# Kernel optimization log

Hardware: AMD Instinct MI355X
Metric: run time of the kernel (lower is better)

## Reference

```python
import jax, jax.numpy as jnp
import numpy as np

B, S, H, DH = 4, 1024, 8, 64
D = H * DH
CLIP_K = 5
NUM_RPR = 2 * CLIP_K + 1  # 11


def setup_inputs() -> dict:
    key = jax.random.key(0)
    ks = jax.random.split(key, 12)
    w_scale = 0.01  # truncated_normal stddev approx
    inp = {
        'q': jax.random.normal(ks[0], (B, S, D), jnp.float32),
        'k': jax.random.normal(ks[1], (B, S, D), jnp.float32),
        'v': jax.random.normal(ks[2], (B, S, D), jnp.float32),
        'rpr_matrix': jax.random.randint(ks[3], (S, S), 0, NUM_RPR, jnp.int32),
        'wq_kernel': jax.random.normal(ks[4], (D, D), jnp.float32) * w_scale,
        'wq_bias': jnp.zeros((D,), jnp.float32),
        'wk_kernel': jax.random.normal(ks[5], (D, D), jnp.float32) * w_scale,
        'wk_bias': jnp.zeros((D,), jnp.float32),
        'wv_kernel': jax.random.normal(ks[6], (D, D), jnp.float32) * w_scale,
        'wv_bias': jnp.zeros((D,), jnp.float32),
        'krpr': jax.random.normal(ks[7], (NUM_RPR, DH), jnp.float32),
    }
    return inp


def reference(q, k, v, rpr_matrix, wq_kernel, wq_bias, wk_kernel, wk_bias,
              wv_kernel, wv_bias, krpr):
    b, s, d = q.shape
    dh = krpr.shape[-1]
    h = d // dh

    def proj(x, w, bias):
        # [B,S,D] -> [B,H,S,DH]
        y = x.reshape(-1, d) @ w + bias
        return y.reshape(b, s, h, dh).transpose(0, 2, 1, 3)

    qh = proj(q, wq_kernel, wq_bias)
    kh = proj(k, wk_kernel, wk_bias)
    vh = proj(v, wv_kernel, wv_bias)

    # standard QK^T scores
    scores = jnp.einsum('bhqd,bhkd->bhqk', qh, kh)
    # RPR key bias: gather per-relative-position key embeddings (note: original
    # code uses krpr for BOTH the key-side and value-side RPR; vrpr is unused)
    alpha = krpr[rpr_matrix]  # [Sq, Sk, DH]
    scores = scores + jnp.einsum('bhqd,qkd->bhqk', qh, alpha)
    scores = scores / jnp.sqrt(jnp.float32(dh))

    probs = jax.nn.softmax(scores, axis=-1)

    ctx = jnp.einsum('bhqk,bhkd->bhqd', probs, vh)
    ctx = ctx + jnp.einsum('bhqk,qkd->bhqd', probs, alpha)

    # [B,H,S,DH] -> [B,S,D]
    return ctx.transpose(0, 2, 1, 3).reshape(b, s, d)
```

## Files before the change

### kernel.cpp

```cpp
#include <hip/hip_runtime.h>

typedef unsigned short u16;
typedef unsigned int u32;
typedef __attribute__((ext_vector_type(8))) short short8;
typedef __attribute__((ext_vector_type(4))) float f32x4;

__device__ __forceinline__ float bf2f(u16 v) {
  return __uint_as_float(((unsigned)v) << 16);
}
__device__ __forceinline__ u16 f2bf(float f) {
  unsigned u = __float_as_uint(f);
  return (u16)((u + 0x7fffu + ((u >> 16) & 1u)) >> 16);
}
__device__ __forceinline__ u32 pk2(float lo, float hi) {
  return (u32)f2bf(lo) | ((u32)f2bf(hi) << 16);
}

__device__ __forceinline__ float ld1in(const void* p, size_t i, bool f32) {
  return f32 ? ((const float*)p)[i] : bf2f(((const u16*)p)[i]);
}
__device__ __forceinline__ float4 ld4in(const void* p, size_t i, bool f32) {
  if (f32) return *(const float4*)((const float*)p + i);
  ushort4 u = *(const ushort4*)((const u16*)p + i);
  return make_float4(bf2f(u.x), bf2f(u.y), bf2f(u.z), bf2f(u.w));
}
__device__ __forceinline__ void ld8in(const void* p, size_t i, bool f32, float* v) {
  if (f32) {
    float4 a = *(const float4*)((const float*)p + i);
    float4 b = *(const float4*)((const float*)p + i + 4);
    v[0] = a.x; v[1] = a.y; v[2] = a.z; v[3] = a.w;
    v[4] = b.x; v[5] = b.y; v[6] = b.z; v[7] = b.w;
  } else {
    ushort4 a = *(const ushort4*)((const u16*)p + i);
    ushort4 b = *(const ushort4*)((const u16*)p + i + 4);
    v[0] = bf2f(a.x); v[1] = bf2f(a.y); v[2] = bf2f(a.z); v[3] = bf2f(a.w);
    v[4] = bf2f(b.x); v[5] = bf2f(b.y); v[6] = bf2f(b.z); v[7] = bf2f(b.w);
  }
}

__device__ __forceinline__ void st1ws(float* p, size_t i, float v) { p[i] = v; }
__device__ __forceinline__ void st1ws(u16* p, size_t i, float v) { p[i] = f2bf(v); }
__device__ __forceinline__ float4 ld4ws(const float* p, size_t i) { return *(const float4*)(p + i); }
__device__ __forceinline__ float4 ld4ws(const u16* p, size_t i) {
  ushort4 u = *(const ushort4*)(p + i);
  return make_float4(bf2f(u.x), bf2f(u.y), bf2f(u.z), bf2f(u.w));
}
template <typename WT>
__device__ __forceinline__ uint4 ld8ws_pk(const WT* p, size_t i) {
  float4 a = ld4ws(p, i), b = ld4ws(p, i + 4);
  uint4 r;
  r.x = pk2(a.x, a.y); r.y = pk2(a.z, a.w);
  r.z = pk2(b.x, b.y); r.w = pk2(b.z, b.w);
  return r;
}
template <>
__device__ __forceinline__ uint4 ld8ws_pk<u16>(const u16* p, size_t i) {
  return *(const uint4*)(p + i);
}


__global__ void rpr_detect_kernel(const u16* __restrict__ q, int* __restrict__ flag) {
  __shared__ int cnt[256];
  int t = threadIdx.x, c = 0;
  for (int i = t; i < 8192; i += 256) {
    unsigned e = (q[i] >> 7) & 0xff;
    c += (e >= 0xC0) ? 1 : 0;
  }
  cnt[t] = c;
  __syncthreads();
  if (t == 0) {
    int s = 0;
    for (int i = 0; i < 256; ++i) s += cnt[i];
    *flag = (s > 128) ? 1 : 0;
  }
}

template <typename WT>
__global__ __launch_bounds__(256, 2) void rpr_proj_mfma(
    const void* __restrict__ xq, const void* __restrict__ xk, const void* __restrict__ xv,
    const void* __restrict__ wqp, const void* __restrict__ wkp, const void* __restrict__ wvp,
    const void* __restrict__ bqp, const void* __restrict__ bkp, const void* __restrict__ bvp,
    WT* __restrict__ ws, const int* __restrict__ flagp) {
  const bool f32 = (*flagp != 0);
  const int z = blockIdx.z;
  const void* __restrict__ X = (z == 0) ? xq : (z == 1) ? xk : xv;
  const void* __restrict__ W = (z == 0) ? wqp : (z == 1) ? wkp : wvp;
  const void* __restrict__ Bb = (z == 0) ? bqp : (z == 1) ? bkp : bvp;
  WT* __restrict__ O = ws + (size_t)z * (4096u * 512u);

  __shared__ u32 as32[64][20];
  __shared__ u32 bs32[64][20];

  const int t = threadIdx.x;
  const int wvi = t >> 6, lane = t & 63;
  const int quad = lane >> 4, col = lane & 15;
  const int m0 = blockIdx.y * 64, n0 = blockIdx.x * 64;

  f32x4 acc[4] = {{0.f, 0.f, 0.f, 0.f}, {0.f, 0.f, 0.f, 0.f},
                  {0.f, 0.f, 0.f, 0.f}, {0.f, 0.f, 0.f, 0.f}};

  for (int k0 = 0; k0 < 512; k0 += 32) {
    {
      int m = t >> 2, kc = (t & 3) * 8;
      float v[8];
      ld8in(X, (size_t)(m0 + m) * 512 + k0 + kc, f32, v);
      uint4 pk;
      pk.x = pk2(v[0], v[1]); pk.y = pk2(v[2], v[3]);
      pk.z = pk2(v[4], v[5]); pk.w = pk2(v[6], v[7]);
      *(uint4*)&as32[m][(t & 3) * 4] = pk;
    }
    {
      int kp = t & 15, nb = (t >> 4) * 4;
      float4 r0 = ld4in(W, (size_t)(k0 + 2 * kp) * 512 + n0 + nb, f32);
      float4 r1 = ld4in(W, (size_t)(k0 + 2 * kp + 1) * 512 + n0 + nb, f32);
      bs32[nb + 0][kp] = pk2(r0.x, r1.x);
      bs32[nb + 1][kp] = pk2(r0.y, r1.y);
      bs32[nb + 2][kp] = pk2(r0.z, r1.z);
      bs32[nb + 3][kp] = pk2(r0.w, r1.w);
    }
    __syncthreads();
    short8 aF = *(const short8*)((const u16*)&as32[wvi * 16 + col][0] + quad * 8);
#pragma unroll
    for (int c = 0; c < 4; ++c) {
      short8 bF = *(const short8*)((const u16*)&bs32[c * 16 + col][0] + quad * 8);
      acc[c] = __builtin_amdgcn_mfma_f32_16x16x32_bf16(aF, bF, acc[c], 0, 0, 0);
    }
    __syncthreads();
  }

  const int h = blockIdx.x;
#pragma unroll
  for (int c = 0; c < 4; ++c) {
    float bias = ld1in(Bb, (size_t)(n0 + c * 16 + col), f32);
#pragma unroll
    for (int reg = 0; reg < 4; ++reg) {
      int m = m0 + wvi * 16 + quad * 4 + reg;
      int bb = m >> 10, s = m & 1023;
      st1ws(O, ((size_t)((bb * 8 + h) * 1024 + s)) * 64 + c * 16 + col,
            acc[c][reg] + bias);
    }
  }
}

template <typename WT>
__global__ __launch_bounds__(256, 2) void rpr_attn_mfma(
    const WT* __restrict__ qkv, const int* __restrict__ rpr,
    const void* __restrict__ krpr, void* __restrict__ out,
    const int* __restrict__ flagp) {
  const bool f32 = (*flagp != 0);
  const int bh = blockIdx.y, q0 = blockIdx.x * 64;
  const int b = bh >> 3, h = bh & 7;
  const WT* __restrict__ qh = qkv + (size_t)bh * 65536;
  const WT* __restrict__ kh = qkv + (size_t)(32 + bh) * 65536;
  const WT* __restrict__ vh = qkv + (size_t)(64 + bh) * 65536;

  __shared__ u16 qs[64][72];
  __shared__ u16 ks[64][72];
  __shared__ u32 vs32[64][36];
  __shared__ u16 ps[4][16][72];
  __shared__ float krl[11][64];
  __shared__ float qrpr[64][12];
  __shared__ int rprt[64][68];

  const int t = threadIdx.x;
  const int wvi = t >> 6, lane = t & 63;
  const int quad = lane >> 4, col = lane & 15;

  for (int i = t; i < 704; i += 256)
    krl[i >> 6][i & 63] = f32 ? ((const float*)krpr)[i] : bf2f(((const u16*)krpr)[i]);
  {
    int r = t >> 2, c = (t & 3) * 16;
    size_t base = (size_t)(q0 + r) * 64 + c;
    *(uint4*)&qs[r][c] = ld8ws_pk(qh, base);
    *(uint4*)&qs[r][c + 8] = ld8ws_pk(qh, base + 8);
  }
  __syncthreads();
  {
    int r = t >> 2, rb = t & 3;
    float d0 = 0.f, d1 = 0.f, d2 = 0.f;
    for (int d = 0; d < 64; ++d) {
      float qv = bf2f(qs[r][d]);
      d0 = fmaf(qv, krl[rb][d], d0);
      d1 = fmaf(qv, krl[rb + 4][d], d1);
      if (rb < 3) d2 = fmaf(qv, krl[rb + 8][d], d2);
    }
    qrpr[r][rb] = d0;
    qrpr[r][rb + 4] = d1;
    if (rb < 3) qrpr[r][rb + 8] = d2;
  }
  short8 qA0, qA1;
  {
    const u16* qrow = &qs[wvi * 16 + col][0];
    qA0 = *(const short8*)(qrow + quad * 8);
    qA1 = *(const short8*)(qrow + 32 + quad * 8);
  }

  float l_part[4] = {0.f, 0.f, 0.f, 0.f};
  float bins[4][11] = {};
  f32x4 ctx[4] = {{0.f, 0.f, 0.f, 0.f}, {0.f, 0.f, 0.f, 0.f},
                  {0.f, 0.f, 0.f, 0.f}, {0.f, 0.f, 0.f, 0.f}};

  for (int kt = 0; kt < 16; ++kt) {
    const int k0 = kt * 64;
    {
      int r = t >> 2, c = (t & 3) * 16;
      size_t base = (size_t)(k0 + r) * 64 + c;
      *(uint4*)&ks[r][c] = ld8ws_pk(kh, base);
      *(uint4*)&ks[r][c + 8] = ld8ws_pk(kh, base + 8);
    }
    {
      int kp = t & 31, dg = t >> 5;
      size_t base = (size_t)(k0 + 2 * kp) * 64 + dg * 8;
      float4 a0 = ld4ws(vh, base), a1 = ld4ws(vh, base + 4);
      float4 b0 = ld4ws(vh, base + 64), b1 = ld4ws(vh, base + 68);
      int d = dg * 8;
      vs32[d + 0][kp] = pk2(a0.x, b0.x);
      vs32[d + 1][kp] = pk2(a0.y, b0.y);
      vs32[d + 2][kp] = pk2(a0.z, b0.z);
      vs32[d + 3][kp] = pk2(a0.w, b0.w);
      vs32[d + 4][kp] = pk2(a1.x, b1.x);
      vs32[d + 5][kp] = pk2(a1.y, b1.y);
      vs32[d + 6][kp] = pk2(a1.z, b1.z);
      vs32[d + 7][kp] = pk2(a1.w, b1.w);
    }
    {
      int rr = t >> 4, cc = (t & 15) * 4;
#pragma unroll
      for (int i = 0; i < 4; ++i) {
        int4 rv = *(const int4*)(rpr + (size_t)(q0 + rr + 16 * i) * 1024 + k0 + cc);
        *(int4*)&rprt[rr + 16 * i][cc] = rv;
      }
    }
    __syncthreads();

    f32x4 sc[4];
    int rid[4][4];
#pragma unroll
    for (int c = 0; c < 4; ++c) {
      const u16* kb = &ks[c * 16 + col][0];
      short8 kB0 = *(const short8*)(kb + quad * 8);
      short8 kB1 = *(const short8*)(kb + 32 + quad * 8);
      f32x4 a = {0.f, 0.f, 0.f, 0.f};
      a = __builtin_amdgcn_mfma_f32_16x16x32_bf16(qA0, kB0, a, 0, 0, 0);
      a = __builtin_amdgcn_mfma_f32_16x16x32_bf16(qA1, kB1, a, 0, 0, 0);
#pragma unroll
      for (int reg = 0; reg < 4; ++reg) {
        int row = wvi * 16 + quad * 4 + reg;
        int id = rprt[row][c * 16 + col];
        rid[c][reg] = id;
        a[reg] = (a[reg] + qrpr[row][id]) * 0.125f;
      }
      sc[c] = a;
    }
#pragma unroll
    for (int c = 0; c < 4; ++c) {
#pragma unroll
      for (int reg = 0; reg < 4; ++reg) {
        float p = __expf(sc[c][reg]);
        l_part[reg] += p;
#pragma unroll
        for (int r = 0; r < 11; ++r) bins[reg][r] += (rid[c][reg] == r) ? p : 0.f;
        ps[wvi][quad * 4 + reg][c * 16 + col] = f2bf(p);
      }
    }
    __syncthreads();

    short8 pA0, pA1;
    {
      const u16* prow = &ps[wvi][col][0];
      pA0 = *(const short8*)(prow + quad * 8);
      pA1 = *(const short8*)(prow + 32 + quad * 8);
    }
#pragma unroll
    for (int c = 0; c < 4; ++c) {
      const u16* vrow = (const u16*)&vs32[c * 16 + col][0];
      short8 vB0 = *(const short8*)(vrow + quad * 8);
      short8 vB1 = *(const short8*)(vrow + 32 + quad * 8);
      ctx[c] = __builtin_amdgcn_mfma_f32_16x16x32_bf16(pA0, vB0, ctx[c], 0, 0, 0);
      ctx[c] = __builtin_amdgcn_mfma_f32_16x16x32_bf16(pA1, vB1, ctx[c], 0, 0, 0);
    }
    __syncthreads();
  }

#pragma unroll
  for (int off = 1; off < 16; off <<= 1) {
#pragma unroll
    for (int reg = 0; reg < 4; ++reg) {
      l_part[reg] += __shfl_xor(l_part[reg], off);
#pragma unroll
      for (int r = 0; r < 11; ++r) bins[reg][r] += __shfl_xor(bins[reg][r], off);
    }
  }
#pragma unroll
  for (int reg = 0; reg < 4; ++reg) {
    int row = wvi * 16 + quad * 4 + reg;
    float inv = 1.f / l_part[reg];
#pragma unroll
    for (int c = 0; c < 4; ++c) {
      float v = ctx[c][reg];
#pragma unroll
      for (int r = 0; r < 11; ++r) v = fmaf(bins[reg][r], krl[r][c * 16 + col], v);
      size_t oidx = (size_t)(b * 1024 + q0 + row) * 512 + h * 64 + c * 16 + col;
      if (f32) ((float*)out)[oidx] = v * inv;
      else ((u16*)out)[oidx] = f2bf(v * inv);
    }
  }
}

extern "C" void kernel_launch(void* const* d_in, const int* in_sizes, int n_in,
                              void* d_out, int out_size, void* d_ws, size_t ws_size,
                              hipStream_t stream) {
  const void* q = d_in[0];
  const void* k = d_in[1];
  const void* v = d_in[2];
  const int* rpr = (const int*)d_in[3];
  const void* wq = d_in[4];
  const void* bq = d_in[5];
  const void* wk = d_in[6];
  const void* bk = d_in[7];
  const void* wv = d_in[8];
  const void* bv = d_in[9];
  const void* krpr = d_in[10];

  int* flag = (int*)d_ws;
  void* wsbase = (void*)((char*)d_ws + 1024);
  const size_t wselems = 3ull * 32 * 1024 * 64;

  rpr_detect_kernel<<<1, 256, 0, stream>>>((const u16*)q, flag);

  if (ws_size >= 1024 + wselems * 4) {
    float* ws = (float*)wsbase;
    rpr_proj_mfma<float><<<dim3(8, 64, 3), 256, 0, stream>>>(
        q, k, v, wq, wk, wv, bq, bk, bv, ws, flag);
    rpr_attn_mfma<float><<<dim3(16, 32), 256, 0, stream>>>(
        ws, rpr, krpr, d_out, flag);
  } else {
    u16* ws = (u16*)wsbase;
    rpr_proj_mfma<u16><<<dim3(8, 64, 3), 256, 0, stream>>>(
        q, k, v, wq, wk, wv, bq, bk, bv, ws, flag);
    rpr_attn_mfma<u16><<<dim3(16, 32), 256, 0, stream>>>(
        ws, rpr, krpr, d_out, flag);
  }
}
```

Baseline: 213.6 us.

## Double-buffer K/V tiles with register prefetch and read rpr indices directly

K and V shared-memory tiles become double-buffered. The next tile's global loads are issued into registers at the top of each iteration and written to the other buffer after the PV MFMAs, which removes one barrier per iteration and overlaps load latency with compute. The rpr index tile is no longer staged through shared memory; each lane reads its indices straight from global memory. V packing now works on packed bf16 words instead of converting from float. This adds register pressure, and the direct rpr reads are strided, uncoalesced global loads.

After: 204.6 us. -4.2%, faster.

```diff
diff --git a/kernel.cpp b/kernel.cpp
--- a/kernel.cpp
+++ b/kernel.cpp
@@ -6,10 +6,10 @@
 typedef __attribute__((ext_vector_type(4))) float f32x4;
 
 __device__ __forceinline__ float bf2f(u16 v) {
-  return __uint_as_float(((unsigned)v) << 16);
+  return __uint_as_float(((u32)v) << 16);
 }
 __device__ __forceinline__ u16 f2bf(float f) {
-  unsigned u = __float_as_uint(f);
+  u32 u = __float_as_uint(f);
   return (u16)((u + 0x7fffu + ((u >> 16) & 1u)) >> 16);
 }
 __device__ __forceinline__ u32 pk2(float lo, float hi) {
@@ -155,24 +155,39 @@
   const WT* __restrict__ vh = qkv + (size_t)(64 + bh) * 65536;
 
   __shared__ u16 qs[64][72];
-  __shared__ u16 ks[64][72];
-  __shared__ u32 vs32[64][36];
+  __shared__ u16 ks[2][64][72];
+  __shared__ u32 vs32[2][64][36];
   __shared__ u16 ps[4][16][72];
   __shared__ float krl[11][64];
   __shared__ float qrpr[64][12];
-  __shared__ int rprt[64][68];
 
   const int t = threadIdx.x;
   const int wvi = t >> 6, lane = t & 63;
   const int quad = lane >> 4, col = lane & 15;
+  const int sr = t >> 2, sc4 = (t & 3) * 16;
+  const int kp = t & 31, dg = (t >> 5) * 8;
 
   for (int i = t; i < 704; i += 256)
     krl[i >> 6][i & 63] = f32 ? ((const float*)krpr)[i] : bf2f(((const u16*)krpr)[i]);
   {
-    int r = t >> 2, c = (t & 3) * 16;
-    size_t base = (size_t)(q0 + r) * 64 + c;
-    *(uint4*)&qs[r][c] = ld8ws_pk(qh, base);
-    *(uint4*)&qs[r][c + 8] = ld8ws_pk(qh, base + 8);
+    size_t base = (size_t)(q0 + sr) * 64 + sc4;
+    *(uint4*)&qs[sr][sc4] = ld8ws_pk(qh, base);
+    *(uint4*)&qs[sr][sc4 + 8] = ld8ws_pk(qh, base + 8);
+  }
+  {
+    size_t kb = (size_t)sr * 64 + sc4;
+    *(uint4*)&ks[0][sr][sc4] = ld8ws_pk(kh, kb);
+    *(uint4*)&ks[0][sr][sc4 + 8] = ld8ws_pk(kh, kb + 8);
+    size_t vb = (size_t)(2 * kp) * 64 + dg;
+    uint4 va = ld8ws_pk(vh, vb), vbb = ld8ws_pk(vh, vb + 64);
+    vs32[0][dg + 0][kp] = (va.x & 0xffffu) | (vbb.x << 16);
+    vs32[0][dg + 1][kp] = (va.x >> 16) | (vbb.x & 0xffff0000u);
+    vs32[0][dg + 2][kp] = (va.y & 0xffffu) | (vbb.y << 16);
+    vs32[0][dg + 3][kp] = (va.y >> 16) | (vbb.y & 0xffff0000u);
+    vs32[0][dg + 4][kp] = (va.z & 0xffffu) | (vbb.z << 16);
+    vs32[0][dg + 5][kp] = (va.z >> 16) | (vbb.z & 0xffff0000u);
+    vs32[0][dg + 6][kp] = (va.w & 0xffffu) | (vbb.w << 16);
+    vs32[0][dg + 7][kp] = (va.w >> 16) | (vbb.w & 0xffff0000u);
   }
   __syncthreads();
   {
@@ -194,6 +209,7 @@
     qA0 = *(const short8*)(qrow + quad * 8);
     qA1 = *(const short8*)(qrow + 32 + quad * 8);
   }
+  __syncthreads();
 
   float l_part[4] = {0.f, 0.f, 0.f, 0.f};
   float bins[4][11] = {};
@@ -201,62 +217,42 @@
                   {0.f, 0.f, 0.f, 0.f}, {0.f, 0.f, 0.f, 0.f}};
 
   for (int kt = 0; kt < 16; ++kt) {
-    const int k0 = kt * 64;
+    const int cur = kt & 1;
+    uint4 pk0, pk1, pva, pvb;
+    if (kt < 15) {
+      size_t kb = (size_t)((kt + 1) * 64 + sr) * 64 + sc4;
+      pk0 = ld8ws_pk(kh, kb);
+      pk1 = ld8ws_pk(kh, kb + 8);
+      size_t vb = (size_t)((kt + 1) * 64 + 2 * kp) * 64 + dg;
+      pva = ld8ws_pk(vh, vb);
+      pvb = ld8ws_pk(vh, vb + 64);
+    }
+    int rid[4][4];
     {
-      int r = t >> 2, c = (t & 3) * 16;
-      size_t base = (size_t)(k0 + r) * 64 + c;
-      *(uint4*)&ks[r][c] = ld8ws_pk(kh, base);
-      *(uint4*)&ks[r][c + 8] = ld8ws_pk(kh, base + 8);
-    }
-    {
-      int kp = t & 31, dg = t >> 5;
-      size_t base = (size_t)(k0 + 2 * kp) * 64 + dg * 8;
-      float4 a0 = ld4ws(vh, base), a1 = ld4ws(vh, base + 4);
-      float4 b0 = ld4ws(vh, base + 64), b1 = ld4ws(vh, base + 68);
-      int d = dg * 8;
-      vs32[d + 0][kp] = pk2(a0.x, b0.x);
-      vs32[d + 1][kp] = pk2(a0.y, b0.y);
-      vs32[d + 2][kp] = pk2(a0.z, b0.z);
-      vs32[d + 3][kp] = pk2(a0.w, b0.w);
-      vs32[d + 4][kp] = pk2(a1.x, b1.x);
-      vs32[d + 5][kp] = pk2(a1.y, b1.y);
-      vs32[d + 6][kp] = pk2(a1.z, b1.z);
-      vs32[d + 7][kp] = pk2(a1.w, b1.w);
-    }
-    {
-      int rr = t >> 4, cc = (t & 15) * 4;
-#pragma unroll
-      for (int i = 0; i < 4; ++i) {
-        int4 rv = *(const int4*)(rpr + (size_t)(q0 + rr + 16 * i) * 1024 + k0 + cc);
-        *(int4*)&rprt[rr + 16 * i][cc] = rv;
-      }
-    }
-    __syncthreads();
-
+      const int* rbase =
+          rpr + (size_t)(q0 + wvi * 16 + quad * 4) * 1024 + kt * 64 + col;
+#pragma unroll
+      for (int reg = 0; reg < 4; ++reg)
+#pragma unroll
+        for (int c = 0; c < 4; ++c) rid[c][reg] = rbase[reg * 1024 + c * 16];
+    }
     f32x4 sc[4];
-    int rid[4][4];
-#pragma unroll
-    for (int c = 0; c < 4; ++c) {
-      const u16* kb = &ks[c * 16 + col][0];
+#pragma unroll
+    for (int c = 0; c < 4; ++c) {
+      const u16* kb = &ks[cur][c * 16 + col][0];
       short8 kB0 = *(const short8*)(kb + quad * 8);
       short8 kB1 = *(const short8*)(kb + 32 + quad * 8);
       f32x4 a = {0.f, 0.f, 0.f, 0.f};
       a = __builtin_amdgcn_mfma_f32_16x16x32_bf16(qA0, kB0, a, 0, 0, 0);
       a = __builtin_amdgcn_mfma_f32_16x16x32_bf16(qA1, kB1, a, 0, 0, 0);
+      sc[c] = a;
+    }
+#pragma unroll
+    for (int c = 0; c < 4; ++c) {
 #pragma unroll
       for (int reg = 0; reg < 4; ++reg) {
         int row = wvi * 16 + quad * 4 + reg;
-        int id = rprt[row][c * 16 + col];
-        rid[c][reg] = id;
-        a[reg] = (a[reg] + qrpr[row][id]) * 0.125f;
-      }
-      sc[c] = a;
-    }
-#pragma unroll
-    for (int c = 0; c < 4; ++c) {
-#pragma unroll
-      for (int reg = 0; reg < 4; ++reg) {
-        float p = __expf(sc[c][reg]);
+        float p = __expf((sc[c][reg] + qrpr[row][rid[c][reg]]) * 0.125f);
         l_part[reg] += p;
 #pragma unroll
         for (int r = 0; r < 11; ++r) bins[reg][r] += (rid[c][reg] == r) ? p : 0.f;
@@ -273,11 +269,23 @@
     }
 #pragma unroll
     for (int c = 0; c < 4; ++c) {
-      const u16* vrow = (const u16*)&vs32[c * 16 + col][0];
+      const u16* vrow = (const u16*)&vs32[cur][c * 16 + col][0];
       short8 vB0 = *(const short8*)(vrow + quad * 8);
       short8 vB1 = *(const short8*)(vrow + 32 + quad * 8);
       ctx[c] = __builtin_amdgcn_mfma_f32_16x16x32_bf16(pA0, vB0, ctx[c], 0, 0, 0);
       ctx[c] = __builtin_amdgcn_mfma_f32_16x16x32_bf16(pA1, vB1, ctx[c], 0, 0, 0);
+    }
+    if (kt < 15) {
+      *(uint4*)&ks[1 - cur][sr][sc4] = pk0;
+      *(uint4*)&ks[1 - cur][sr][sc4 + 8] = pk1;
+      vs32[1 - cur][dg + 0][kp] = (pva.x & 0xffffu) | (pvb.x << 16);
+      vs32[1 - cur][dg + 1][kp] = (pva.x >> 16) | (pvb.x & 0xffff0000u);
+      vs32[1 - cur][dg + 2][kp] = (pva.y & 0xffffu) | (pvb.y << 16);
+      vs32[1 - cur][dg + 3][kp] = (pva.y >> 16) | (pvb.y & 0xffff0000u);
+      vs32[1 - cur][dg + 4][kp] = (pva.z & 0xffffu) | (pvb.z << 16);
+      vs32[1 - cur][dg + 5][kp] = (pva.z >> 16) | (pvb.z & 0xffff0000u);
+      vs32[1 - cur][dg + 6][kp] = (pva.w & 0xffffu) | (pvb.w << 16);
+      vs32[1 - cur][dg + 7][kp] = (pva.w >> 16) | (pvb.w & 0xffff0000u);
     }
     __syncthreads();
   }
```
